# Kernel optimization log

Hardware: AMD Instinct MI355X
Metric: run time of the kernel (lower is better)

## Reference

```python
import jax, jax.numpy as jnp
import numpy as np

BN_EPS = 1e-5


def conv3x3(x, w, b):
    # x: [B,C,H,W], w: [O,C,3,3], same padding, stride 1
    y = jax.lax.conv_general_dilated(x, w, (1, 1), ((1, 1), (1, 1)),
                                     dimension_numbers=('NCHW', 'OIHW', 'NCHW'))
    return y + b[None, :, None, None]


def bilinear_sample(x, py, px):
    # x: [B,C,H,W]; py/px: [B,K,H,W] fractional sample coords (zero outside borders)
    B, C, H, W = x.shape
    y0 = jnp.floor(py)
    x0 = jnp.floor(px)
    wy1 = py - y0  # frac weights
    wx1 = px - x0

    def corner(yc, xc, wgt):
        valid = (yc >= 0) & (yc <= H - 1) & (xc >= 0) & (xc <= W - 1)
        yi = jnp.clip(yc, 0, H - 1).astype(jnp.int32)
        xi = jnp.clip(xc, 0, W - 1).astype(jnp.int32)
        # gather per batch: [C,H,W] indexed by [K,H,W] -> [C,K,H,W]
        g = jax.vmap(lambda img, yy, xx: img[:, yy, xx])(x, yi, xi)  # [B,C,K,H,W]
        return g * jnp.where(valid, wgt, 0.0)[:, None]

    return (corner(y0, x0, (1 - wy1) * (1 - wx1))
            + corner(y0, x0 + 1, (1 - wy1) * wx1)
            + corner(y0 + 1, x0, wy1 * (1 - wx1))
            + corner(y0 + 1, x0 + 1, wy1 * wx1))  # [B,C,9,H,W]


def deform_conv(x, conv_w, off_w, off_b, mask_w, mask_b, gamma, beta):
    B, C, H, W = x.shape
    O = conv_w.shape[0]
    offset = conv3x3(x, off_w, off_b)                      # [B,18,H,W]
    mask = jax.nn.sigmoid(conv3x3(x, mask_w, mask_b))      # [B,9,H,W]
    off = offset.reshape(B, 9, 2, H, W)                    # tap k = kh*3+kw, (dy,dx)
    ky = jnp.repeat(jnp.arange(3), 3).astype(x.dtype)      # kernel row per tap
    kx = jnp.tile(jnp.arange(3), 3).astype(x.dtype)        # kernel col per tap
    gy = jnp.arange(H, dtype=x.dtype)
    gx = jnp.arange(W, dtype=x.dtype)
    # sample position = out pos - pad + kernel idx + learned offset
    py = off[:, :, 0] + gy[None, None, :, None] + (ky - 1.0)[None, :, None, None]
    px = off[:, :, 1] + gx[None, None, None, :] + (kx - 1.0)[None, :, None, None]
    val = bilinear_sample(x, py, px)                       # [B,C,9,H,W]
    val = val * mask[:, None]                              # modulated (DCNv2)
    out = jnp.einsum('bckhw,ock->bohw', val, conv_w.reshape(O, C, 9))
    # BatchNorm (training-mode batch stats) + ReLU
    mean = out.mean(axis=(0, 2, 3))
    var = out.var(axis=(0, 2, 3))
    out = (out - mean[None, :, None, None]) * jax.lax.rsqrt(var + BN_EPS)[None, :, None, None]
    out = out * gamma[None, :, None, None] + beta[None, :, None, None]
    return jax.nn.relu(out)


def setup_inputs() -> dict:
    key = jax.random.key(0)
    ks = jax.random.split(key, 8)
    B, Cin, Cout, H, W = 2, 64, 64, 128, 128
    x = jax.random.normal(ks[0], (B, Cin, H, W), dtype=jnp.float32)
    fan = Cin * 9
    conv_w = jax.random.normal(ks[1], (Cout, Cin, 3, 3), dtype=jnp.float32) / np.sqrt(fan)
    # offset/mask convs: small random weights so offsets are non-degenerate but modest
    off_w = jax.random.normal(ks[2], (18, Cin, 3, 3), dtype=jnp.float32) * 0.01
    off_b = jax.random.normal(ks[3], (18,), dtype=jnp.float32) * 0.1
    mask_w = jax.random.normal(ks[4], (9, Cin, 3, 3), dtype=jnp.float32) * 0.01
    mask_b = jnp.zeros((9,), dtype=jnp.float32)
    gamma = jnp.ones((Cout,), dtype=jnp.float32)
    beta = jnp.zeros((Cout,), dtype=jnp.float32)
    return {"x": x, "conv_w": conv_w, "off_w": off_w, "off_b": off_b,
            "mask_w": mask_w, "mask_b": mask_b, "gamma": gamma, "beta": beta}


def reference(x, conv_w, off_w, off_b, mask_w, mask_b, gamma, beta):
    return deform_conv(x, conv_w, off_w, off_b, mask_w, mask_b, gamma, beta)
```

## Files before the change

### kernel.cpp

```cpp
#include <hip/hip_runtime.h>

typedef __attribute__((ext_vector_type(8))) short bf16x8;
typedef __attribute__((ext_vector_type(4))) float f32x4;
typedef unsigned int  u32;
typedef unsigned short u16;

constexpr int B_  = 2;
constexpr int C_  = 64;
constexpr int O_  = 64;
constexpr int H_  = 128;
constexpr int W_  = 128;
constexpr int HW_ = H_ * W_;
constexpr int NPIX_ = B_ * HW_;
constexpr float BN_EPS_ = 1e-5f;

__device__ __forceinline__ u16 f2bf(float f) {
    u32 u = __float_as_uint(f);
    u = (u + 0x7fffu + ((u >> 16) & 1u)) >> 16;
    return (u16)u;
}
__device__ __forceinline__ float bflo(u32 u) { return __uint_as_float(u << 16); }
__device__ __forceinline__ float bfhi(u32 u) { return __uint_as_float(u & 0xffff0000u); }

__global__ __launch_bounds__(256)
void prep_kernel(const float* __restrict__ x, const float* __restrict__ conv_w,
                 const float* __restrict__ off_w, const float* __restrict__ mask_w,
                 u16* __restrict__ xt, u16* __restrict__ WpF, u16* __restrict__ W27F) {
    int bid = blockIdx.x, tid = threadIdx.x;
    if (bid < 512) {
        __shared__ u16 tile[64][66];
        int b = bid >> 8;
        int hw0 = (bid & 255) * 64;
        int c = tid >> 2, pq = (tid & 3) * 16;
        const float* src = x + (((size_t)(b * 64 + c)) << 14) + hw0 + pq;
#pragma unroll
        for (int i = 0; i < 4; i++) {
            float4 v = *(const float4*)(src + i * 4);
            tile[pq + i * 4 + 0][c] = f2bf(v.x);
            tile[pq + i * 4 + 1][c] = f2bf(v.y);
            tile[pq + i * 4 + 2][c] = f2bf(v.z);
            tile[pq + i * 4 + 3][c] = f2bf(v.w);
        }
        __syncthreads();
        int p = tid >> 2, cs = (tid & 3) * 16;
        uint4* dst = (uint4*)(xt + (((size_t)(b << 14)) + hw0 + p) * 64 + cs);
        dst[0] = *(const uint4*)&tile[p][cs];
        dst[1] = *(const uint4*)&tile[p][cs + 8];
    } else if (bid < 512 + 144) {
        int i = (bid - 512) * 256 + tid;
        int j = i & 7, lane = (i >> 3) & 63, t = (i >> 9) & 3, s = i >> 11;
        int o = t * 16 + (lane & 15);
        int kk = s * 32 + (lane >> 4) * 8 + j;
        int tap = kk >> 6, c = kk & 63;
        WpF[i] = f2bf(conv_w[(o * 64 + c) * 9 + tap]);
    } else if (bid < 512 + 144 + 72) {
        int i = (bid - 656) * 256 + tid;
        int j = i & 7, lane = (i >> 3) & 63, t = (i >> 9) & 1, s = i >> 10;
        int row = t * 16 + (lane & 15);
        int kk = s * 32 + (lane >> 4) * 8 + j;
        int tap = kk >> 6, c = kk & 63;
        float v = 0.f;
        if (row < 18) v = off_w[(row * 64 + c) * 9 + tap];
        else if (row < 27) v = mask_w[((row - 18) * 64 + c) * 9 + tap];
        W27F[i] = f2bf(v);
    } else {
        if (tid < 64) xt[((u32)NPIX_ << 6) + tid] = 0;
    }
}

template<int TAP>
__device__ __forceinline__ void metaA(int h, int w, u32 bb, u32 qoff, u32& abase) {
    constexpr int dh = TAP / 3 - 1, dw = TAP % 3 - 1;
    int hh = h + dh, ww = w + dw;
    bool valid = (hh >= 0) && (hh < H_) && (ww >= 0) && (ww < W_);
    u32 idx = valid ? (bb + (u32)(hh * W_ + ww)) : (u32)NPIX_;
    abase = (idx << 6) + qoff;
}

template<int SG>
__device__ __forceinline__ void mfma2(const u16* __restrict__ W27F, int lane,
                                      const bf16x8& sv, f32x4 (&acc)[2]) {
#pragma unroll
    for (int t = 0; t < 2; t++) {
        bf16x8 af = *(const bf16x8*)(W27F + (u32)((SG * 2 + t) * 64 + lane) * 8u);
        acc[t] = __builtin_amdgcn_mfma_f32_16x16x32_bf16(af, sv, acc[t], 0, 0, 0);
    }
}

template<int KH>
__device__ __forceinline__ void runA(const u16* __restrict__ xt,
                                     const u16* __restrict__ W27F,
                                     int h, int w, u32 bb, u32 qoff, int lane,
                                     f32x4 (&acc)[2]) {
    u32 a0, a1, a2;
    metaA<3 * KH + 0>(h, w, bb, qoff, a0);
    metaA<3 * KH + 1>(h, w, bb, qoff, a1);
    metaA<3 * KH + 2>(h, w, bb, qoff, a2);
    bf16x8 s0 = *(const bf16x8*)(xt + a0);
    bf16x8 s1 = *(const bf16x8*)(xt + a0 + 32);
    bf16x8 s2 = *(const bf16x8*)(xt + a1);
    bf16x8 s3 = *(const bf16x8*)(xt + a1 + 32);
    bf16x8 s4 = *(const bf16x8*)(xt + a2);
    bf16x8 s5 = *(const bf16x8*)(xt + a2 + 32);
    mfma2<6 * KH + 0>(W27F, lane, s0, acc);
    mfma2<6 * KH + 1>(W27F, lane, s1, acc);
    mfma2<6 * KH + 2>(W27F, lane, s2, acc);
    mfma2<6 * KH + 3>(W27F, lane, s3, acc);
    mfma2<6 * KH + 4>(W27F, lane, s4, acc);
    mfma2<6 * KH + 5>(W27F, lane, s5, acc);
}

template<int TAP>
__device__ __forceinline__ void metaB(const float* __restrict__ moff,
                                      const float* __restrict__ mmask,
                                      int p32, int h, int w, u32 bb, u32 qoff,
                                      u32 (&qc)[4], float (&cw)[4]) {
    float dy = moff[(2 * TAP) * 32 + p32];
    float dx = moff[(2 * TAP + 1) * 32 + p32];
    float m  = mmask[TAP * 32 + p32];
    constexpr float kdy = (float)(TAP / 3 - 1), kdx = (float)(TAP % 3 - 1);
    float py = dy + (float)h + kdy;
    float px = dx + (float)w + kdx;
    float y0 = floorf(py), x0 = floorf(px);
    float ly = py - y0, lx = px - x0, hy = 1.f - ly, hx = 1.f - lx;
    float y1 = y0 + 1.f, x1 = x0 + 1.f;
    bool vy0 = (y0 >= 0.f) && (y0 <= 127.f);
    bool vy1 = (y1 >= 0.f) && (y1 <= 127.f);
    bool vx0 = (x0 >= 0.f) && (x0 <= 127.f);
    bool vx1 = (x1 >= 0.f) && (x1 <= 127.f);
    int iy0 = (int)fminf(fmaxf(y0, 0.f), 127.f);
    int iy1 = (int)fminf(fmaxf(y1, 0.f), 127.f);
    int ix0 = (int)fminf(fmaxf(x0, 0.f), 127.f);
    int ix1 = (int)fminf(fmaxf(x1, 0.f), 127.f);
    qc[0] = ((bb + (u32)(iy0 * W_ + ix0)) << 6) + qoff; cw[0] = (vy0 && vx0) ? hy * hx * m : 0.f;
    qc[1] = ((bb + (u32)(iy0 * W_ + ix1)) << 6) + qoff; cw[1] = (vy0 && vx1) ? hy * lx * m : 0.f;
    qc[2] = ((bb + (u32)(iy1 * W_ + ix0)) << 6) + qoff; cw[2] = (vy1 && vx0) ? ly * hx * m : 0.f;
    qc[3] = ((bb + (u32)(iy1 * W_ + ix1)) << 6) + qoff; cw[3] = (vy1 && vx1) ? ly * lx * m : 0.f;
}

__device__ __forceinline__ void ld4(const u16* __restrict__ xt, const u32 (&qc)[4],
                                    u32 sc, uint4 (&p)[4]) {
#pragma unroll
    for (int i = 0; i < 4; i++) p[i] = *(const uint4*)(xt + qc[i] + sc);
}

__device__ __forceinline__ bf16x8 cmb(const uint4 (&p)[4], const float (&cw)[4]) {
    const u32* p0 = &p[0].x; const u32* p1 = &p[1].x;
    const u32* p2 = &p[2].x; const u32* p3 = &p[3].x;
    bf16x8 sv;
#pragma unroll
    for (int i = 0; i < 4; i++) {
        float lo = cw[0] * bflo(p0[i]) + cw[1] * bflo(p1[i])
                 + cw[2] * bflo(p2[i]) + cw[3] * bflo(p3[i]);
        float hi = cw[0] * bfhi(p0[i]) + cw[1] * bfhi(p1[i])
                 + cw[2] * bfhi(p2[i]) + cw[3] * bfhi(p3[i]);
        sv[2 * i]     = (short)f2bf(lo);
        sv[2 * i + 1] = (short)f2bf(hi);
    }
    return sv;
}

template<int SG>
__device__ __forceinline__ void mfma4(const u16* __restrict__ WpF, int lane,
                                      const bf16x8& sv, f32x4 (&acc)[4]) {
#pragma unroll
    for (int t = 0; t < 4; t++) {
        bf16x8 af = *(const bf16x8*)(WpF + (u32)((SG * 4 + t) * 64 + lane) * 8u);
        acc[t] = __builtin_amdgcn_mfma_f32_16x16x32_bf16(af, sv, acc[t], 0, 0, 0);
    }
}

template<int KH>
__device__ __forceinline__ void runB(const u16* __restrict__ xt,
                                     const float* __restrict__ moff,
                                     const float* __restrict__ mmask,
                                     const u16* __restrict__ WpF,
                                     int p32, int h, int w, u32 bb, u32 qoff,
                                     int lane, f32x4 (&acc)[4]) {
    u32 q0[4], q1[4], q2[4]; float w0[4], w1[4], w2[4];
    metaB<3 * KH + 0>(moff, mmask, p32, h, w, bb, qoff, q0, w0);
    metaB<3 * KH + 1>(moff, mmask, p32, h, w, bb, qoff, q1, w1);
    metaB<3 * KH + 2>(moff, mmask, p32, h, w, bb, qoff, q2, w2);
    uint4 pA[4], pB[4], pC[4];
    ld4(xt, q0, 0,  pA);
    ld4(xt, q0, 32, pB);
    ld4(xt, q1, 0,  pC);
    bf16x8 sv;
    sv = cmb(pA, w0); mfma4<6 * KH + 0>(WpF, lane, sv, acc); ld4(xt, q1, 32, pA);
    sv = cmb(pB, w0); mfma4<6 * KH + 1>(WpF, lane, sv, acc); ld4(xt, q2, 0,  pB);
    sv = cmb(pC, w1); mfma4<6 * KH + 2>(WpF, lane, sv, acc); ld4(xt, q2, 32, pC);
    sv = cmb(pA, w1); mfma4<6 * KH + 3>(WpF, lane, sv, acc);
    sv = cmb(pB, w2); mfma4<6 * KH + 4>(WpF, lane, sv, acc);
    sv = cmb(pC, w2); mfma4<6 * KH + 5>(WpF, lane, sv, acc);
}

__global__ __launch_bounds__(384, 3)
void gemm_ab_kernel(const u16* __restrict__ xt, const u16* __restrict__ W27F,
                    const u16* __restrict__ WpF,
                    const float* __restrict__ off_b, const float* __restrict__ mask_b,
                    u16* __restrict__ pre16, float* __restrict__ part) {
    __shared__ float red[4][64][17];
    __shared__ float moff[18 * 32];
    __shared__ float mmask[9 * 32];
    const int tid = threadIdx.x;
    const int lane = tid & 63, wv = tid >> 6;
    const int ph = wv & 1, kh = wv >> 1;
    const int quad = lane >> 4, r = lane & 15;
    const int pbase = blockIdx.x * 32;
    const int b = pbase >> 14, hwb = pbase & (HW_ - 1);
    const int p32 = ph * 16 + r;
    const int hw = hwb + p32, h = hw >> 7, w = hw & (W_ - 1);
    const u32 bb = (u32)b << 14;
    const u32 qoff = (u32)quad * 8u;

    {
        f32x4 acc[2];
        acc[0] = (f32x4){0.f, 0.f, 0.f, 0.f};
        acc[1] = (f32x4){0.f, 0.f, 0.f, 0.f};
        if (kh == 0)      runA<0>(xt, W27F, h, w, bb, qoff, lane, acc);
        else if (kh == 1) runA<1>(xt, W27F, h, w, bb, qoff, lane, acc);
        else              runA<2>(xt, W27F, h, w, bb, qoff, lane, acc);

        if (kh != 0) {
            int slot = (kh - 1) * 2 + ph;
#pragma unroll
            for (int t = 0; t < 2; t++)
#pragma unroll
                for (int g = 0; g < 4; g++) red[slot][lane][t * 4 + g] = acc[t][g];
        }
        __syncthreads();
        if (kh == 0) {
#pragma unroll
            for (int t = 0; t < 2; t++) {
#pragma unroll
                for (int g = 0; g < 4; g++) {
                    float v = acc[t][g] + red[ph][lane][t * 4 + g] + red[2 + ph][lane][t * 4 + g];
                    int o = t * 16 + quad * 4 + g;
                    if (o < 18) {
                        moff[o * 32 + p32] = v + off_b[o];
                    } else if (o < 27) {
                        v += mask_b[o - 18];
                        mmask[(o - 18) * 32 + p32] = 1.f / (1.f + __expf(-v));
                    }
                }
            }
        }
        __syncthreads();
    }

    f32x4 acc[4];
#pragma unroll
    for (int t = 0; t < 4; t++) acc[t] = (f32x4){0.f, 0.f, 0.f, 0.f};

    if (kh == 0)      runB<0>(xt, moff, mmask, WpF, p32, h, w, bb, qoff, lane, acc);
    else if (kh == 1) runB<1>(xt, moff, mmask, WpF, p32, h, w, bb, qoff, lane, acc);
    else              runB<2>(xt, moff, mmask, WpF, p32, h, w, bb, qoff, lane, acc);

    if (kh != 0) {
        int slot = (kh - 1) * 2 + ph;
#pragma unroll
        for (int t = 0; t < 4; t++)
#pragma unroll
            for (int g = 0; g < 4; g++) red[slot][lane][t * 4 + g] = acc[t][g];
    }
    __syncthreads();
    if (kh == 0) {
        const u32 slot = (u32)blockIdx.x * 2 + (u32)ph;
#pragma unroll
        for (int t = 0; t < 4; t++) {
#pragma unroll
            for (int g = 0; g < 4; g++) {
                float v = acc[t][g] + red[ph][lane][t * 4 + g] + red[2 + ph][lane][t * 4 + g];
                int o = t * 16 + quad * 4 + g;
                pre16[(u32)(b * 64 + o) * HW_ + hw] = f2bf(v);
                float s = v, s2 = v * v;
#pragma unroll
                for (int off = 8; off >= 1; off >>= 1) {
                    s  += __shfl_down(s, off, 16);
                    s2 += __shfl_down(s2, off, 16);
                }
                if (r == 0) {
                    part[(u32)o * 2048 + slot] = s;
                    part[131072 + (u32)o * 2048 + slot] = s2;
                }
            }
        }
    }
}

__global__ __launch_bounds__(256)
void stats_red_kernel(const float* __restrict__ part, float* __restrict__ stats) {
    __shared__ float p4[4];
    int i = blockIdx.x;
    const float* src = part + (u32)(i >> 6) * 131072 + (u32)(i & 63) * 2048;
    float s = 0.f;
    for (int rr = threadIdx.x; rr < 2048; rr += 256) s += src[rr];
#pragma unroll
    for (int off = 32; off >= 1; off >>= 1) s += __shfl_down(s, off);
    if ((threadIdx.x & 63) == 0) p4[threadIdx.x >> 6] = s;
    __syncthreads();
    if (threadIdx.x == 0) stats[i] = p4[0] + p4[1] + p4[2] + p4[3];
}

__global__ __launch_bounds__(256)
void bn_relu_kernel(const u16* __restrict__ pre16, const float* __restrict__ stats,
                    const float* __restrict__ gamma, const float* __restrict__ beta,
                    float* __restrict__ out) {
    int i4 = blockIdx.x * 256 + threadIdx.x;
    int ch = (i4 >> 12) & (O_ - 1);
    float mean = stats[ch] * (1.f / NPIX_);
    float var  = stats[64 + ch] * (1.f / NPIX_) - mean * mean;
    float scale = gamma[ch] * rsqrtf(var + BN_EPS_);
    float shift = beta[ch] - mean * scale;
    uint2 v = ((const uint2*)pre16)[i4];
    float4 o;
    o.x = fmaxf(fmaf(bflo(v.x), scale, shift), 0.f);
    o.y = fmaxf(fmaf(bfhi(v.x), scale, shift), 0.f);
    o.z = fmaxf(fmaf(bflo(v.y), scale, shift), 0.f);
    o.w = fmaxf(fmaf(bfhi(v.y), scale, shift), 0.f);
    ((float4*)out)[i4] = o;
}

extern "C" void kernel_launch(void* const* d_in, const int* in_sizes, int n_in,
                              void* d_out, int out_size, void* d_ws, size_t ws_size,
                              hipStream_t stream) {
    const float* x      = (const float*)d_in[0];
    const float* conv_w = (const float*)d_in[1];
    const float* off_w  = (const float*)d_in[2];
    const float* off_b  = (const float*)d_in[3];
    const float* mask_w = (const float*)d_in[4];
    const float* mask_b = (const float*)d_in[5];
    const float* gamma  = (const float*)d_in[6];
    const float* beta   = (const float*)d_in[7];
    float* out = (float*)d_out;

    char* ws = (char*)d_ws;
    u16*  xt     = (u16*)(ws);
    u16*  pre16  = (u16*)(ws + 4194432);
    u16*  WpF    = (u16*)(ws + 8388736);
    u16*  W27F   = (u16*)(ws + 8462464);
    float* part  = (float*)(ws + 8499328);
    float* stats = (float*)(ws + 9547904);

    prep_kernel<<<729, 256, 0, stream>>>(x, conv_w, off_w, mask_w, xt, WpF, W27F);
    gemm_ab_kernel<<<NPIX_ / 32, 384, 0, stream>>>(xt, W27F, WpF, off_b, mask_b, pre16, part);
    stats_red_kernel<<<128, 256, 0, stream>>>(part, stats);
    bn_relu_kernel<<<2048, 256, 0, stream>>>(pre16, stats, gamma, beta, out);
}
```

Baseline: 122.7 us.

## Switch sampling and MFMA path from bf16 to fp16 with packed half2 bilinear combine

Converts the input, conv and offset/mask weights to fp16 instead of bf16 and uses fp16 MFMA instructions. The bilinear combine now runs in packed half2 FMAs instead of unpacking to fp32 and rounding back to bf16, which cuts ALU work per sample. The load order in the deformable pass is reshuffled so the first halves of all three taps are fetched before the second halves. Launch bounds drop from 3 to 2 waves-per-EU hint, which allows more registers per thread at the cost of occupancy. Accumulating in fp16 and the narrower fp16 range add some precision risk for the bilinear combine.

```diff
diff --git a/kernel.cpp b/kernel.cpp
--- a/kernel.cpp
+++ b/kernel.cpp
@@ -1,7 +1,9 @@
 #include <hip/hip_runtime.h>
-
-typedef __attribute__((ext_vector_type(8))) short bf16x8;
+#include <hip/hip_fp16.h>
+
+typedef __attribute__((ext_vector_type(8))) _Float16 f16x8;
 typedef __attribute__((ext_vector_type(4))) float f32x4;
+typedef __attribute__((ext_vector_type(4))) unsigned int u32x4;
 typedef unsigned int  u32;
 typedef unsigned short u16;
 
@@ -21,6 +23,7 @@
 }
 __device__ __forceinline__ float bflo(u32 u) { return __uint_as_float(u << 16); }
 __device__ __forceinline__ float bfhi(u32 u) { return __uint_as_float(u & 0xffff0000u); }
+__device__ __forceinline__ u16 f2h(float f) { return __half_as_ushort(__float2half(f)); }
 
 __global__ __launch_bounds__(256)
 void prep_kernel(const float* __restrict__ x, const float* __restrict__ conv_w,
@@ -36,10 +39,10 @@
 #pragma unroll
         for (int i = 0; i < 4; i++) {
             float4 v = *(const float4*)(src + i * 4);
-            tile[pq + i * 4 + 0][c] = f2bf(v.x);
-            tile[pq + i * 4 + 1][c] = f2bf(v.y);
-            tile[pq + i * 4 + 2][c] = f2bf(v.z);
-            tile[pq + i * 4 + 3][c] = f2bf(v.w);
+            tile[pq + i * 4 + 0][c] = f2h(v.x);
+            tile[pq + i * 4 + 1][c] = f2h(v.y);
+            tile[pq + i * 4 + 2][c] = f2h(v.z);
+            tile[pq + i * 4 + 3][c] = f2h(v.w);
         }
         __syncthreads();
         int p = tid >> 2, cs = (tid & 3) * 16;
@@ -52,7 +55,7 @@
         int o = t * 16 + (lane & 15);
         int kk = s * 32 + (lane >> 4) * 8 + j;
         int tap = kk >> 6, c = kk & 63;
-        WpF[i] = f2bf(conv_w[(o * 64 + c) * 9 + tap]);
+        WpF[i] = f2h(conv_w[(o * 64 + c) * 9 + tap]);
     } else if (bid < 512 + 144 + 72) {
         int i = (bid - 656) * 256 + tid;
         int j = i & 7, lane = (i >> 3) & 63, t = (i >> 9) & 1, s = i >> 10;
@@ -62,7 +65,7 @@
         float v = 0.f;
         if (row < 18) v = off_w[(row * 64 + c) * 9 + tap];
         else if (row < 27) v = mask_w[((row - 18) * 64 + c) * 9 + tap];
-        W27F[i] = f2bf(v);
+        W27F[i] = f2h(v);
     } else {
         if (tid < 64) xt[((u32)NPIX_ << 6) + tid] = 0;
     }
@@ -78,12 +81,12 @@
 }
 
 template<int SG>
-__device__ __forceinline__ void mfma2(const u16* __restrict__ W27F, int lane,
-                                      const bf16x8& sv, f32x4 (&acc)[2]) {
+__device__ __forceinline__ void mfma2h(const u16* __restrict__ W27F, int lane,
+                                       const f16x8& sv, f32x4 (&acc)[2]) {
 #pragma unroll
     for (int t = 0; t < 2; t++) {
-        bf16x8 af = *(const bf16x8*)(W27F + (u32)((SG * 2 + t) * 64 + lane) * 8u);
-        acc[t] = __builtin_amdgcn_mfma_f32_16x16x32_bf16(af, sv, acc[t], 0, 0, 0);
+        f16x8 af = *(const f16x8*)(W27F + (u32)((SG * 2 + t) * 64 + lane) * 8u);
+        acc[t] = __builtin_amdgcn_mfma_f32_16x16x32_f16(af, sv, acc[t], 0, 0, 0);
     }
 }
 
@@ -96,25 +99,25 @@
     metaA<3 * KH + 0>(h, w, bb, qoff, a0);
     metaA<3 * KH + 1>(h, w, bb, qoff, a1);
     metaA<3 * KH + 2>(h, w, bb, qoff, a2);
-    bf16x8 s0 = *(const bf16x8*)(xt + a0);
-    bf16x8 s1 = *(const bf16x8*)(xt + a0 + 32);
-    bf16x8 s2 = *(const bf16x8*)(xt + a1);
-    bf16x8 s3 = *(const bf16x8*)(xt + a1 + 32);
-    bf16x8 s4 = *(const bf16x8*)(xt + a2);
-    bf16x8 s5 = *(const bf16x8*)(xt + a2 + 32);
-    mfma2<6 * KH + 0>(W27F, lane, s0, acc);
-    mfma2<6 * KH + 1>(W27F, lane, s1, acc);
-    mfma2<6 * KH + 2>(W27F, lane, s2, acc);
-    mfma2<6 * KH + 3>(W27F, lane, s3, acc);
-    mfma2<6 * KH + 4>(W27F, lane, s4, acc);
-    mfma2<6 * KH + 5>(W27F, lane, s5, acc);
+    f16x8 s0 = *(const f16x8*)(xt + a0);
+    f16x8 s1 = *(const f16x8*)(xt + a0 + 32);
+    f16x8 s2 = *(const f16x8*)(xt + a1);
+    f16x8 s3 = *(const f16x8*)(xt + a1 + 32);
+    f16x8 s4 = *(const f16x8*)(xt + a2);
+    f16x8 s5 = *(const f16x8*)(xt + a2 + 32);
+    mfma2h<6 * KH + 0>(W27F, lane, s0, acc);
+    mfma2h<6 * KH + 1>(W27F, lane, s1, acc);
+    mfma2h<6 * KH + 2>(W27F, lane, s2, acc);
+    mfma2h<6 * KH + 3>(W27F, lane, s3, acc);
+    mfma2h<6 * KH + 4>(W27F, lane, s4, acc);
+    mfma2h<6 * KH + 5>(W27F, lane, s5, acc);
 }
 
 template<int TAP>
 __device__ __forceinline__ void metaB(const float* __restrict__ moff,
                                       const float* __restrict__ mmask,
                                       int p32, int h, int w, u32 bb, u32 qoff,
-                                      u32 (&qc)[4], float (&cw)[4]) {
+                                      u32 (&qc)[4], __half2 (&cwh)[4]) {
     float dy = moff[(2 * TAP) * 32 + p32];
     float dx = moff[(2 * TAP + 1) * 32 + p32];
     float m  = mmask[TAP * 32 + p32];
@@ -132,10 +135,14 @@
     int iy1 = (int)fminf(fmaxf(y1, 0.f), 127.f);
     int ix0 = (int)fminf(fmaxf(x0, 0.f), 127.f);
     int ix1 = (int)fminf(fmaxf(x1, 0.f), 127.f);
-    qc[0] = ((bb + (u32)(iy0 * W_ + ix0)) << 6) + qoff; cw[0] = (vy0 && vx0) ? hy * hx * m : 0.f;
-    qc[1] = ((bb + (u32)(iy0 * W_ + ix1)) << 6) + qoff; cw[1] = (vy0 && vx1) ? hy * lx * m : 0.f;
-    qc[2] = ((bb + (u32)(iy1 * W_ + ix0)) << 6) + qoff; cw[2] = (vy1 && vx0) ? ly * hx * m : 0.f;
-    qc[3] = ((bb + (u32)(iy1 * W_ + ix1)) << 6) + qoff; cw[3] = (vy1 && vx1) ? ly * lx * m : 0.f;
+    qc[0] = ((bb + (u32)(iy0 * W_ + ix0)) << 6) + qoff;
+    qc[1] = ((bb + (u32)(iy0 * W_ + ix1)) << 6) + qoff;
+    qc[2] = ((bb + (u32)(iy1 * W_ + ix0)) << 6) + qoff;
+    qc[3] = ((bb + (u32)(iy1 * W_ + ix1)) << 6) + qoff;
+    cwh[0] = __float2half2_rn((vy0 && vx0) ? hy * hx * m : 0.f);
+    cwh[1] = __float2half2_rn((vy0 && vx1) ? hy * lx * m : 0.f);
+    cwh[2] = __float2half2_rn((vy1 && vx0) ? ly * hx * m : 0.f);
+    cwh[3] = __float2half2_rn((vy1 && vx1) ? ly * lx * m : 0.f);
 }
 
 __device__ __forceinline__ void ld4(const u16* __restrict__ xt, const u32 (&qc)[4],
@@ -144,29 +151,28 @@
     for (int i = 0; i < 4; i++) p[i] = *(const uint4*)(xt + qc[i] + sc);
 }
 
-__device__ __forceinline__ bf16x8 cmb(const uint4 (&p)[4], const float (&cw)[4]) {
-    const u32* p0 = &p[0].x; const u32* p1 = &p[1].x;
-    const u32* p2 = &p[2].x; const u32* p3 = &p[3].x;
-    bf16x8 sv;
+__device__ __forceinline__ f16x8 cmbH(const uint4 (&p)[4], const __half2 (&cw)[4]) {
+    const u32* a = &p[0].x; const u32* b = &p[1].x;
+    const u32* c = &p[2].x; const u32* d = &p[3].x;
+    u32x4 r;
 #pragma unroll
     for (int i = 0; i < 4; i++) {
-        float lo = cw[0] * bflo(p0[i]) + cw[1] * bflo(p1[i])
-                 + cw[2] * bflo(p2[i]) + cw[3] * bflo(p3[i]);
-        float hi = cw[0] * bfhi(p0[i]) + cw[1] * bfhi(p1[i])
-                 + cw[2] * bfhi(p2[i]) + cw[3] * bfhi(p3[i]);
-        sv[2 * i]     = (short)f2bf(lo);
-        sv[2 * i + 1] = (short)f2bf(hi);
-    }
-    return sv;
+        __half2 t = __hmul2(*(const __half2*)&a[i], cw[0]);
+        t = __hfma2(*(const __half2*)&b[i], cw[1], t);
+        t = __hfma2(*(const __half2*)&c[i], cw[2], t);
+        t = __hfma2(*(const __half2*)&d[i], cw[3], t);
+        r[i] = *(const u32*)&t;
+    }
+    return __builtin_bit_cast(f16x8, r);
 }
 
 template<int SG>
-__device__ __forceinline__ void mfma4(const u16* __restrict__ WpF, int lane,
-                                      const bf16x8& sv, f32x4 (&acc)[4]) {
+__device__ __forceinline__ void mfma4h(const u16* __restrict__ WpF, int lane,
+                                       const f16x8& sv, f32x4 (&acc)[4]) {
 #pragma unroll
     for (int t = 0; t < 4; t++) {
-        bf16x8 af = *(const bf16x8*)(WpF + (u32)((SG * 4 + t) * 64 + lane) * 8u);
-        acc[t] = __builtin_amdgcn_mfma_f32_16x16x32_bf16(af, sv, acc[t], 0, 0, 0);
+        f16x8 af = *(const f16x8*)(WpF + (u32)((SG * 4 + t) * 64 + lane) * 8u);
+        acc[t] = __builtin_amdgcn_mfma_f32_16x16x32_f16(af, sv, acc[t], 0, 0, 0);
     }
 }
 
@@ -177,24 +183,25 @@
                                      const u16* __restrict__ WpF,
                                      int p32, int h, int w, u32 bb, u32 qoff,
                                      int lane, f32x4 (&acc)[4]) {
-    u32 q0[4], q1[4], q2[4]; float w0[4], w1[4], w2[4];
+    u32 q0[4], q1[4], q2[4];
+    __half2 w0[4], w1[4], w2[4];
     metaB<3 * KH + 0>(moff, mmask, p32, h, w, bb, qoff, q0, w0);
     metaB<3 * KH + 1>(moff, mmask, p32, h, w, bb, qoff, q1, w1);
     metaB<3 * KH + 2>(moff, mmask, p32, h, w, bb, qoff, q2, w2);
-    uint4 pA[4], pB[4], pC[4];
-    ld4(xt, q0, 0,  pA);
-    ld4(xt, q0, 32, pB);
-    ld4(xt, q1, 0,  pC);
-    bf16x8 sv;
-    sv = cmb(pA, w0); mfma4<6 * KH + 0>(WpF, lane, sv, acc); ld4(xt, q1, 32, pA);
-    sv = cmb(pB, w0); mfma4<6 * KH + 1>(WpF, lane, sv, acc); ld4(xt, q2, 0,  pB);
-    sv = cmb(pC, w1); mfma4<6 * KH + 2>(WpF, lane, sv, acc); ld4(xt, q2, 32, pC);
-    sv = cmb(pA, w1); mfma4<6 * KH + 3>(WpF, lane, sv, acc);
-    sv = cmb(pB, w2); mfma4<6 * KH + 4>(WpF, lane, sv, acc);
-    sv = cmb(pC, w2); mfma4<6 * KH + 5>(WpF, lane, sv, acc);
-}
-
-__global__ __launch_bounds__(384, 3)
+    uint4 p0[4], p1[4], p2[4];
+    ld4(xt, q0, 0, p0);
+    ld4(xt, q1, 0, p1);
+    ld4(xt, q2, 0, p2);
+    f16x8 sv;
+    sv = cmbH(p0, w0); mfma4h<6 * KH + 0>(WpF, lane, sv, acc); ld4(xt, q0, 32, p0);
+    sv = cmbH(p1, w1); mfma4h<6 * KH + 2>(WpF, lane, sv, acc); ld4(xt, q1, 32, p1);
+    sv = cmbH(p2, w2); mfma4h<6 * KH + 4>(WpF, lane, sv, acc); ld4(xt, q2, 32, p2);
+    sv = cmbH(p0, w0); mfma4h<6 * KH + 1>(WpF, lane, sv, acc);
+    sv = cmbH(p1, w1); mfma4h<6 * KH + 3>(WpF, lane, sv, acc);
+    sv = cmbH(p2, w2); mfma4h<6 * KH + 5>(WpF, lane, sv, acc);
+}
+
+__global__ __launch_bounds__(384, 2)
 void gemm_ab_kernel(const u16* __restrict__ xt, const u16* __restrict__ W27F,
                     const u16* __restrict__ WpF,
                     const float* __restrict__ off_b, const float* __restrict__ mask_b,
```

Result: no change. 124.1 us (+1.1%).
